# Kernel tuning notes

Measured on AMD Instinct MI355X. Metric: run time of the kernel, lower is better.

## Reference

```python
import jax, jax.numpy as jnp
import numpy as np

N = 100000   # number of nodes
H = 512      # n_hidden
K = 128      # number of clusters
BETA = 100.0 # cluster_temp
ALPHA = 0.5
NUM_ITER = 10
EPS = 1e-8


def _cluster(data, mu, cluster_temp, num_iter):
    """Differentiable soft k-means, faithful to cluster() in the torch source."""
    data = data / (jnp.linalg.norm(data, axis=1) + EPS)[:, None]
    dist = data @ mu.T  # placeholder; overwritten in loop (num_iter >= 1)
    for _ in range(num_iter):
        mu = mu / jnp.linalg.norm(mu, axis=1)[:, None]
        dist = data @ mu.T                      # [N, K]
        r = jax.nn.softmax(cluster_temp * dist, axis=1)
        cluster_r = r.sum(axis=0)               # [K]
        mu = (r.T @ data) / cluster_r[:, None]  # diag(1/cluster_r) @ (r.T @ data)
    r = jax.nn.softmax(cluster_temp * dist, axis=1)
    return mu, r


def setup_inputs() -> dict:
    key = jax.random.key(0)
    k1, k2, k3, k4 = jax.random.split(key, 4)
    positive = jax.random.normal(k1, (N, H), dtype=jnp.float32)
    negative = jax.random.normal(k2, (N, H), dtype=jnp.float32)
    init = jax.random.uniform(k3, (K, H), dtype=jnp.float32)  # torch.rand(K, nout)
    bound = 1.0 / np.sqrt(H)
    W = jax.random.uniform(k4, (H, H), dtype=jnp.float32, minval=-bound, maxval=bound)
    return {"positive": positive, "negative": negative, "init": init, "W": W}


def reference(positive, negative, init, W):
    # Clusterator.forward: 10-iter k-means, then 1 more iter from detached means
    mu_init, _ = _cluster(positive, init, BETA, NUM_ITER)
    mu, r = _cluster(positive, jax.lax.stop_gradient(mu_init), BETA, 1)

    graph_summary = jax.nn.sigmoid(positive.mean(axis=0))    # [H]
    cluster_summary = jax.nn.sigmoid(r @ mu)                 # [N, H]

    # Discriminator: features @ (W @ summary)
    Ws = W @ graph_summary                                    # [H]
    pos_graph = positive @ Ws                                 # [N]
    neg_graph = negative @ Ws                                 # [N]

    # BCEWithLogitsLoss with all-ones / all-zeros targets
    bce_ones = lambda x: jnp.mean(jax.nn.softplus(-x))
    bce_zeros = lambda x: jnp.mean(jax.nn.softplus(x))

    l = ALPHA * (bce_ones(pos_graph) + bce_zeros(neg_graph))

    # DiscriminatorK: rowwise dot of features with cluster summary
    pos_cluster = jnp.sum(positive * cluster_summary, axis=1)  # [N]
    neg_cluster = jnp.sum(negative * cluster_summary, axis=1)  # [N]

    l = l + (1.0 - ALPHA) * (bce_ones(pos_cluster) + bce_zeros(neg_cluster))
    return l
```

## Files before the change

### kernel.cpp

```cpp
#include <hip/hip_runtime.h>
#include <math.h>

#define NN 100000
#define PADN 100096
#define NBLK128 782
#define HH 512
#define KK 128
#define BETA 100.0f
#define EPSF 1e-8f
#define ITERS 11
#define NSPLIT 128
#define NCHUNK2 (PADN / 128)
#define PREPB 1024

typedef __attribute__((ext_vector_type(8))) short short8v;
typedef __attribute__((ext_vector_type(4))) float float4v;

typedef const __attribute__((address_space(1))) void* gas_t;
typedef __attribute__((address_space(3))) void* las_t;

__device__ __forceinline__ void gload16(const void* g, void* l) {
  __builtin_amdgcn_global_load_lds((gas_t)g, (las_t)l, 16, 0, 0);
}

__device__ __forceinline__ unsigned short f2bf(float x) {
  unsigned int u = __float_as_uint(x);
  unsigned int r = (u + 0x7fff + ((u >> 16) & 1)) >> 16;
  return (unsigned short)r;
}
__device__ __forceinline__ float bf2f(unsigned short b) {
  return __uint_as_float((unsigned int)b << 16);
}
__device__ __forceinline__ unsigned char f2fp8(float x) {
  return (unsigned char)(__builtin_amdgcn_cvt_pk_fp8_f32(x, x, 0, false) & 0xff);
}
__device__ __forceinline__ float fp82f(unsigned char b) {
  return __builtin_amdgcn_cvt_f32_fp8((unsigned int)b, 0);
}
#define CVT8_FP8(dst, pv)                                      \
  dst[0] = __builtin_amdgcn_cvt_f32_fp8((pv).x, 0);            \
  dst[1] = __builtin_amdgcn_cvt_f32_fp8((pv).x, 1);            \
  dst[2] = __builtin_amdgcn_cvt_f32_fp8((pv).x, 2);            \
  dst[3] = __builtin_amdgcn_cvt_f32_fp8((pv).x, 3);            \
  dst[4] = __builtin_amdgcn_cvt_f32_fp8((pv).y, 0);            \
  dst[5] = __builtin_amdgcn_cvt_f32_fp8((pv).y, 1);            \
  dst[6] = __builtin_amdgcn_cvt_f32_fp8((pv).y, 2);            \
  dst[7] = __builtin_amdgcn_cvt_f32_fp8((pv).y, 3);

__device__ __forceinline__ float wave_reduce_sum(float v) {
#pragma unroll
  for (int off = 32; off > 0; off >>= 1) v += __shfl_xor(v, off);
  return v;
}
__device__ __forceinline__ float softplusf(float x) {
  return fmaxf(x, 0.0f) + log1pf(expf(-fabsf(x)));
}

__global__ void prep_kernel(const float* __restrict__ pos,
                            float* __restrict__ inv_norm,
                            float* __restrict__ colpart,
                            unsigned short* __restrict__ posbb,
                            unsigned char* __restrict__ posb8) {
  int t = threadIdx.x;
  int w = t >> 6, lane = t & 63;
  int gw = blockIdx.x * 4 + w;
  float cpart[8] = {0, 0, 0, 0, 0, 0, 0, 0};
  for (int row = gw; row < NN; row += PREPB * 4) {
    const float* p = pos + (size_t)row * HH + lane * 8;
    float4 f0 = *(const float4*)p;
    float4 f1 = *(const float4*)(p + 4);
    float v[8] = {f0.x, f0.y, f0.z, f0.w, f1.x, f1.y, f1.z, f1.w};
    float ss = 0.f;
#pragma unroll
    for (int u = 0; u < 8; ++u) {
      ss += v[u] * v[u];
      cpart[u] += v[u];
    }
    ss = wave_reduce_sum(ss);
    float inv = 1.0f / (sqrtf(ss) + EPSF);
    if (lane == 0) inv_norm[row] = inv;
    short8v o;
#pragma unroll
    for (int u = 0; u < 8; ++u) o[u] = (short)f2bf(v[u] * inv);
    *(short8v*)&posbb[(size_t)row * HH + lane * 8] = o;
    int p0 = 0, p1 = 0;
    p0 = __builtin_amdgcn_cvt_pk_fp8_f32(v[0] * inv, v[1] * inv, p0, false);
    p0 = __builtin_amdgcn_cvt_pk_fp8_f32(v[2] * inv, v[3] * inv, p0, true);
    p1 = __builtin_amdgcn_cvt_pk_fp8_f32(v[4] * inv, v[5] * inv, p1, false);
    p1 = __builtin_amdgcn_cvt_pk_fp8_f32(v[6] * inv, v[7] * inv, p1, true);
    int2 pk = {p0, p1};
    *(int2*)&posb8[(size_t)row * HH + lane * 8] = pk;
  }
  {
    int idx = blockIdx.x * 256 + t;
    if (idx < (PADN - NN) * HH / 8) {
      short8v z = (short8v){0, 0, 0, 0, 0, 0, 0, 0};
      *(short8v*)&posbb[(size_t)NN * HH + idx * 8] = z;
    }
    if (idx < (PADN - NN) * HH / 16) {
      int4 z4 = {0, 0, 0, 0};
      *(int4*)&posb8[(size_t)NN * HH + idx * 16] = z4;
    }
  }
  __shared__ float cs[HH];
  cs[t] = 0.f;
  cs[t + 256] = 0.f;
  __syncthreads();
#pragma unroll
  for (int u = 0; u < 8; ++u) atomicAdd(&cs[lane * 8 + u], cpart[u]);
  __syncthreads();
  colpart[(size_t)blockIdx.x * HH + t] = cs[t];
  colpart[(size_t)blockIdx.x * HH + t + 256] = cs[t + 256];
}

__launch_bounds__(256)
__global__ void transpose_kernel(const unsigned short* __restrict__ posbb,
                                 unsigned char* __restrict__ posbT8) {
  __shared__ unsigned short tile[64][72];
  int t = threadIdx.x;
  int i0 = blockIdx.x * 64, h0 = blockIdx.y * 64;
  int r = t >> 2, cq = (t & 3) * 16;
#pragma unroll
  for (int q = 0; q < 2; ++q) {
    short8v v = *(const short8v*)&posbb[(size_t)(i0 + r) * HH + h0 + cq + q * 8];
#pragma unroll
    for (int e = 0; e < 8; ++e) tile[cq + q * 8 + e][r] = (unsigned short)v[e];
  }
  __syncthreads();
  int h = t >> 2, iq = (t & 3) * 16;
  const unsigned short* src = &tile[h][iq];
  int o[4];
#pragma unroll
  for (int q = 0; q < 4; ++q) {
    int pk = 0;
    pk = __builtin_amdgcn_cvt_pk_fp8_f32(bf2f(src[q * 4 + 0]), bf2f(src[q * 4 + 1]), pk, false);
    pk = __builtin_amdgcn_cvt_pk_fp8_f32(bf2f(src[q * 4 + 2]), bf2f(src[q * 4 + 3]), pk, true);
    o[q] = pk;
  }
  int4 ov = {o[0], o[1], o[2], o[3]};
  *(int4*)&posbT8[(size_t)(h0 + h) * PADN + i0 + iq] = ov;
}

__global__ void gs_kernel(const float* __restrict__ colpart, float* __restrict__ gs) {
  int t = threadIdx.x;
  float s = 0.f;
  for (int b = 0; b < PREPB; ++b) s += colpart[(size_t)b * HH + t];
  float m = s * (1.0f / NN);
  gs[t] = 1.0f / (1.0f + expf(-m));
}

__global__ void wsum_kernel(const float* __restrict__ W, const float* __restrict__ gs,
                            float* __restrict__ Ws) {
  int w = threadIdx.x >> 6, lane = threadIdx.x & 63;
  int row = blockIdx.x * 4 + w;
  const float* Wr = W + (size_t)row * HH;
  float s = 0.f;
#pragma unroll
  for (int j = 0; j < 8; ++j) s += Wr[lane + 64 * j] * gs[lane + 64 * j];
  s = wave_reduce_sum(s);
  if (lane == 0) Ws[row] = s;
}

__global__ void norm_mu_kernel(const float* __restrict__ src, unsigned char* __restrict__ mub8) {
  int k = blockIdx.x, t = threadIdx.x;
  float v0 = src[k * HH + t], v1 = src[k * HH + t + 256];
  float ss = v0 * v0 + v1 * v1;
  ss = wave_reduce_sum(ss);
  __shared__ float red[4];
  if ((t & 63) == 0) red[t >> 6] = ss;
  __syncthreads();
  float inv = 1.0f / sqrtf(red[0] + red[1] + red[2] + red[3]);
  mub8[k * HH + t] = f2fp8(v0 * inv);
  mub8[k * HH + t + 256] = f2fp8(v1 * inv);
}

__launch_bounds__(256, 4)
__global__ void dist_mfma(const unsigned char* __restrict__ posb8,
                          const unsigned char* __restrict__ mub8,
                          unsigned char* __restrict__ rbf8,
                          unsigned char* __restrict__ rbfT8,
                          float* __restrict__ crblk,
                          int write_rbf) {
  __shared__ __align__(16) unsigned char smem[32768];
  unsigned char* As0 = smem;
  unsigned char* Bs0 = smem + 16384;
  unsigned char* rT8 = smem;
  __shared__ float redM[2][128];
  __shared__ float redS[2][128];
  __shared__ float crS[2][128];

  int t = threadIdx.x;
  int w = t >> 6, l = t & 63;
  int wr = w >> 1, wc = w & 1;
  int i0 = blockIdx.x * 128;

  float4v acc[4][4];
#pragma unroll
  for (int mi = 0; mi < 4; ++mi)
#pragma unroll
    for (int ni = 0; ni < 4; ++ni) acc[mi][ni] = (float4v){0.f, 0.f, 0.f, 0.f};

  int rsub = l >> 2;
  int sslot = ((l & 3) ^ (rsub & 3)) << 4;

  auto stage = [&](int buf, int ch) {
    int h0 = ch * 64;
#pragma unroll
    for (int j = 0; j < 2; ++j) {
      int v = w * 2 + j;
      int row = v * 16 + rsub;
      gload16(posb8 + (size_t)(i0 + row) * HH + h0 + sslot, As0 + buf * 8192 + v * 1024);
      gload16(mub8 + (size_t)row * HH + h0 + sslot, Bs0 + buf * 8192 + v * 1024);
    }
  };

  stage(0, 0);
  int cur = 0;
  int g = l >> 4;
  int half8 = (g & 1) * 8;
  for (int ch = 0; ch < 8; ++ch) {
    if (ch < 7) {
      stage(cur ^ 1, ch + 1);
      asm volatile("s_waitcnt vmcnt(4)" ::: "memory");
    } else {
      asm volatile("s_waitcnt vmcnt(0)" ::: "memory");
    }
    __builtin_amdgcn_s_barrier();
    __builtin_amdgcn_sched_barrier(0);
    const char* ab = (const char*)(As0 + cur * 8192);
    const char* bb = (const char*)(Bs0 + cur * 8192);
#pragma unroll
    for (int ks = 0; ks < 2; ++ks) {
      long af[4], bfr[4];
      int slot16 = ks * 2 + (g >> 1);
      int soff = ((slot16 ^ (l & 3)) << 4) + half8;
#pragma unroll
      for (int mi = 0; mi < 4; ++mi) {
        int row = wr * 64 + mi * 16 + (l & 15);
        af[mi] = *(const long*)(ab + row * 64 + soff);
      }
#pragma unroll
      for (int ni = 0; ni < 4; ++ni) {
        int row = wc * 64 + ni * 16 + (l & 15);
        bfr[ni] = *(const long*)(bb + row * 64 + soff);
      }
#pragma unroll
      for (int mi = 0; mi < 4; ++mi)
#pragma unroll
        for (int ni = 0; ni < 4; ++ni)
          acc[mi][ni] = __builtin_amdgcn_mfma_f32_16x16x32_fp8_fp8(af[mi], bfr[ni], acc[mi][ni], 0, 0, 0);
    }
    __builtin_amdgcn_sched_barrier(0);
    __builtin_amdgcn_s_barrier();
    __builtin_amdgcn_sched_barrier(0);
    cur ^= 1;
  }

  float wmax[4][4];
#pragma unroll
  for (int mi = 0; mi < 4; ++mi)
#pragma unroll
    for (int j = 0; j < 4; ++j) {
      float m = fmaxf(fmaxf(acc[mi][0][j], acc[mi][1][j]), fmaxf(acc[mi][2][j], acc[mi][3][j])) * BETA;
      m = fmaxf(m, __shfl_xor(m, 1));
      m = fmaxf(m, __shfl_xor(m, 2));
      m = fmaxf(m, __shfl_xor(m, 4));
      m = fmaxf(m, __shfl_xor(m, 8));
      wmax[mi][j] = m;
    }
  if ((l & 15) == 0) {
#pragma unroll
    for (int mi = 0; mi < 4; ++mi)
#pragma unroll
      for (int j = 0; j < 4; ++j)
        redM[wc][wr * 64 + mi * 16 + (l >> 4) * 4 + j] = wmax[mi][j];
  }
  __syncthreads();
  float fm[4][4];
#pragma unroll
  for (int mi = 0; mi < 4; ++mi)
#pragma unroll
    for (int j = 0; j < 4; ++j) {
      int row = wr * 64 + mi * 16 + (l >> 4) * 4 + j;
      fm[mi][j] = fmaxf(redM[0][row], redM[1][row]);
    }
#pragma unroll
  for (int mi = 0; mi < 4; ++mi)
#pragma unroll
    for (int j = 0; j < 4; ++j) {
      float s = 0.f;
#pragma unroll
      for (int ni = 0; ni < 4; ++ni) {
        float e = __expf(acc[mi][ni][j] * BETA - fm[mi][j]);
        acc[mi][ni][j] = e;
        s += e;
      }
      s += __shfl_xor(s, 1);
      s += __shfl_xor(s, 2);
      s += __shfl_xor(s, 4);
      s += __shfl_xor(s, 8);
      wmax[mi][j] = s;
    }
  if ((l & 15) == 0) {
#pragma unroll
    for (int mi = 0; mi < 4; ++mi)
#pragma unroll
      for (int j = 0; j < 4; ++j)
        redS[wc][wr * 64 + mi * 16 + (l >> 4) * 4 + j] = wmax[mi][j];
  }
  __syncthreads();

  float cpart[4] = {0.f, 0.f, 0.f, 0.f};
#pragma unroll
  for (int mi = 0; mi < 4; ++mi)
#pragma unroll
    for (int j = 0; j < 4; ++j) {
      int row = wr * 64 + mi * 16 + (l >> 4) * 4 + j;
      float invs = 1.0f / (redS[0][row] + redS[1][row]);
      bool valid = (i0 + row) < NN;
#pragma unroll
      for (int ni = 0; ni < 4; ++ni) {
        unsigned char q8 = f2fp8(acc[mi][ni][j] * invs);
        if (valid) cpart[ni] += fp82f(q8);
        rT8[(wc * 64 + ni * 16 + (l & 15)) * 144 + row] = q8;
      }
    }
#pragma unroll
  for (int ni = 0; ni < 4; ++ni) {
    float c = cpart[ni];
    c += __shfl_xor(c, 16);
    c += __shfl_xor(c, 32);
    if (l < 16) crS[wr][wc * 64 + ni * 16 + l] = c;
  }
  __syncthreads();
  if (t < 128) crblk[(size_t)blockIdx.x * KK + t] = crS[0][t] + crS[1][t];

  {
    int c = t >> 1, half = t & 1;
    const unsigned char* src = &rT8[c * 144 + half * 64];
    unsigned char* dst = &rbfT8[(size_t)c * PADN + i0 + half * 64];
#pragma unroll
    for (int q = 0; q < 4; ++q)
      *(short8v*)(dst + q * 16) = *(const short8v*)(src + q * 16);
  }
  if (write_rbf) {
    int i = t >> 1, chalf = t & 1;
#pragma unroll
    for (int q = 0; q < 8; ++q) {
      unsigned int lo = 0, hi = 0;
#pragma unroll
      for (int e = 0; e < 4; ++e)
        lo |= ((unsigned int)rT8[(chalf * 64 + q * 8 + e) * 144 + i]) << (8 * e);
#pragma unroll
      for (int e = 0; e < 4; ++e)
        hi |= ((unsigned int)rT8[(chalf * 64 + q * 8 + 4 + e) * 144 + i]) << (8 * e);
      uint2 pk = {lo, hi};
      *(uint2*)&rbf8[(size_t)(i0 + i) * KK + chalf * 64 + q * 8] = pk;
    }
  }
}

__launch_bounds__(256, 2)
__global__ void muup_mfma(const unsigned char* __restrict__ rbfT8,
                          const unsigned char* __restrict__ posbT8,
                          unsigned short* __restrict__ part) {
  __shared__ __align__(16) unsigned char smem[65536];
  unsigned char* As0 = smem;
  unsigned char* Bs0 = smem + 32768;
  int t = threadIdx.x;
  int w = t >> 6, l = t & 63;
  int wr = w >> 1, wc = w & 1;
  int ht = blockIdx.x, s = blockIdx.y;

  float4v acc[4][4];
#pragma unroll
  for (int mi = 0; mi < 4; ++mi)
#pragma unroll
    for (int ni = 0; ni < 4; ++ni) acc[mi][ni] = (float4v){0.f, 0.f, 0.f, 0.f};

  int rsub = l >> 3;
  int sslot = ((l & 7) ^ rsub) << 4;

  auto stage = [&](int buf, int ch) {
    size_t ib = (size_t)ch * 128;
#pragma unroll
    for (int j = 0; j < 4; ++j) {
      int v = w * 4 + j;
      int row = v * 8 + rsub;
      gload16(rbfT8 + (size_t)row * PADN + ib + sslot, As0 + buf * 16384 + v * 1024);
      gload16(posbT8 + (size_t)(ht * 128 + row) * PADN + ib + sslot, Bs0 + buf * 16384 + v * 1024);
    }
  };

  int ch = s;
  stage(0, ch);
  int cur = 0;
  int g = l >> 4;
  int half8 = (g & 1) * 8;
  for (; ch < NCHUNK2; ch += NSPLIT) {
    int nxt = ch + NSPLIT;
    if (nxt < NCHUNK2) {
      stage(cur ^ 1, nxt);
      asm volatile("s_waitcnt vmcnt(8)" ::: "memory");
    } else {
      asm volatile("s_waitcnt vmcnt(0)" ::: "memory");
    }
    __builtin_amdgcn_s_barrier();
    __builtin_amdgcn_sched_barrier(0);
    const char* ab = (const char*)(As0 + cur * 16384);
    const char* bb = (const char*)(Bs0 + cur * 16384);
#pragma unroll
    for (int ks = 0; ks < 4; ++ks) {
      long af[4], bfr[4];
      int slot16 = ks * 2 + (g >> 1);
#pragma unroll
      for (int mi = 0; mi < 4; ++mi) {
        int row = wr * 64 + mi * 16 + (l & 15);
        af[mi] = *(const long*)(ab + row * 128 + ((slot16 ^ (l & 7)) << 4) + half8);
      }
#pragma unroll
      for (int ni = 0; ni < 4; ++ni) {
        int row = wc * 64 + ni * 16 + (l & 15);
        bfr[ni] = *(const long*)(bb + row * 128 + ((slot16 ^ (l & 7)) << 4) + half8);
      }
#pragma unroll
      for (int mi = 0; mi < 4; ++mi)
#pragma unroll
        for (int ni = 0; ni < 4; ++ni)
          acc[mi][ni] = __builtin_amdgcn_mfma_f32_16x16x32_fp8_fp8(af[mi], bfr[ni], acc[mi][ni], 0, 0, 0);
    }
    __builtin_amdgcn_sched_barrier(0);
    __builtin_amdgcn_s_barrier();
    __builtin_amdgcn_sched_barrier(0);
    cur ^= 1;
  }
#pragma unroll
  for (int mi = 0; mi < 4; ++mi)
#pragma unroll
    for (int ni = 0; ni < 4; ++ni)
#pragma unroll
      for (int j = 0; j < 4; ++j) {
        int c = wr * 64 + mi * 16 + (l >> 4) * 4 + j;
        int hh = wc * 64 + ni * 16 + (l & 15);
        part[((size_t)s * KK + c) * HH + ht * 128 + hh] = f2bf(acc[mi][ni][j]);
      }
}

__global__ void finorm_kernel(const unsigned short* __restrict__ part,
                              const float* __restrict__ crblk,
                              unsigned char* __restrict__ mub8,
                              unsigned char* __restrict__ mubT8, int write_mubT) {
  int c = blockIdx.x, t = threadIdx.x;
  __shared__ float credL[4];
  float crp = 0.f;
  for (int b = t; b < NBLK128; b += 256) crp += crblk[(size_t)b * KK + c];
  crp = wave_reduce_sum(crp);
  if ((t & 63) == 0) credL[t >> 6] = crp;
  __syncthreads();
  float cr = credL[0] + credL[1] + credL[2] + credL[3];
  float inv = 1.0f / cr;
  float s0 = 0.f, s1 = 0.f;
  const unsigned short* pb = part + (size_t)c * HH;
#pragma unroll 4
  for (int s2 = 0; s2 < NSPLIT; ++s2) {
    s0 += bf2f(pb[(size_t)s2 * KK * HH + t]);
    s1 += bf2f(pb[(size_t)s2 * KK * HH + t + 256]);
  }
  float v0 = s0 * inv, v1 = s1 * inv;
  if (write_mubT) {
    mubT8[(size_t)t * KK + c] = f2fp8(v0);
    mubT8[(size_t)(t + 256) * KK + c] = f2fp8(v1);
  }
  float ss = v0 * v0 + v1 * v1;
  ss = wave_reduce_sum(ss);
  __shared__ float red[4];
  if ((t & 63) == 0) red[t >> 6] = ss;
  __syncthreads();
  float rn = 1.0f / sqrtf(red[0] + red[1] + red[2] + red[3]);
  mub8[c * HH + t] = f2fp8(v0 * rn);
  mub8[c * HH + t + 256] = f2fp8(v1 * rn);
}

__launch_bounds__(512, 4)
__global__ void loss_mfma(const unsigned char* __restrict__ rbf8,
                          const unsigned char* __restrict__ mubT8,
                          const unsigned char* __restrict__ posb8,
                          const float* __restrict__ neg,
                          const float* __restrict__ inv_norm,
                          const float* __restrict__ Wsv, float* __restrict__ loss_accum) {
  __shared__ __align__(16) unsigned char rS8[128 * 128];
  __shared__ __align__(16) unsigned char BsU8[128 * 144];
  __shared__ float WsS[HH];
  __shared__ float pcS[128], ncS[128], pgS[128], ngS[128];
  int t = threadIdx.x;
  int w = t >> 6, l = t & 63;
  int wr = w >> 1, wc = w & 1;
  int i0 = blockIdx.x * 128;

  int rsub = l >> 3;
  int sslot = ((l & 7) ^ rsub) << 4;
  {
    const unsigned char* gb = rbf8 + (size_t)i0 * KK;
#pragma unroll
    for (int j = 0; j < 2; ++j) {
      int v = w * 2 + j;
      int row = v * 8 + rsub;
      gload16(gb + (size_t)row * KK + sslot, rS8 + v * 1024);
    }
  }
  WsS[t] = Wsv[t];
  if (t < 128) {
    pcS[t] = 0.f; ncS[t] = 0.f; pgS[t] = 0.f; ngS[t] = 0.f;
  }

  int g = l >> 4;
  int half8 = (g & 1) * 8;
  for (int p = 0; p < 4; ++p) {
    __syncthreads();
    {
      const unsigned char* gb = mubT8 + (size_t)p * 128 * KK;
#pragma unroll
      for (int j = 0; j < 2; ++j) {
        int v = w * 2 + j;
        int row = v * 8 + rsub;
        gload16(gb + (size_t)row * KK + sslot, BsU8 + v * 1024);
      }
    }
    __syncthreads();

    float4v acc[2][4];
#pragma unroll
    for (int mi = 0; mi < 2; ++mi)
#pragma unroll
      for (int ni = 0; ni < 4; ++ni) acc[mi][ni] = (float4v){0.f, 0.f, 0.f, 0.f};

#pragma unroll
    for (int ks = 0; ks < 4; ++ks) {
      long af[2], bfr[4];
      int slot16 = ks * 2 + (g >> 1);
      int soff = ((slot16 ^ (l & 7)) << 4) + half8;
#pragma unroll
      for (int mi = 0; mi < 2; ++mi) {
        int row = wr * 32 + mi * 16 + (l & 15);
        af[mi] = *(const long*)((const char*)rS8 + row * 128 + soff);
      }
#pragma unroll
      for (int ni = 0; ni < 4; ++ni) {
        int hrow = wc * 64 + ni * 16 + (l & 15);
        bfr[ni] = *(const long*)((const char*)BsU8 + hrow * 128 + soff);
      }
#pragma unroll
      for (int mi = 0; mi < 2; ++mi)
#pragma unroll
        for (int ni = 0; ni < 4; ++ni)
          acc[mi][ni] = __builtin_amdgcn_mfma_f32_16x16x32_fp8_fp8(af[mi], bfr[ni], acc[mi][ni], 0, 0, 0);
    }
    __syncthreads();

    unsigned char* csS = BsU8;
#pragma unroll
    for (int mi = 0; mi < 2; ++mi)
#pragma unroll
      for (int ni = 0; ni < 4; ++ni)
#pragma unroll
        for (int j = 0; j < 4; ++j) {
          int row = wr * 32 + mi * 16 + (l >> 4) * 4 + j;
          int col = wc * 64 + ni * 16 + (l & 15);
          csS[row * 144 + col] = f2fp8(1.0f / (1.0f + __expf(-acc[mi][ni][j])));
        }
    __syncthreads();

    {
      int rl = t >> 2;
      int q = t & 3;
      int gi = i0 + rl;
      bool valid = gi < NN;
      float pc = 0.f, nc = 0.f, pg = 0.f, ng = 0.f;
      const unsigned char* pr = posb8 + (size_t)gi * HH + p * 128;
      const float* nr = neg + (size_t)gi * HH + p * 128;
      const unsigned char* cr = csS + rl * 144;
#pragma unroll
      for (int e = 0; e < 4; ++e) {
        int cb = e * 32 + q * 8;
        uint2 cs8 = *(const uint2*)(cr + cb);
        if (valid) {
          uint2 pv8 = *(const uint2*)(pr + cb);
          float4 nv0 = *(const float4*)(nr + cb);
          float4 nv1 = *(const float4*)(nr + cb + 4);
          float sf[8], pf[8];
          CVT8_FP8(sf, cs8)
          CVT8_FP8(pf, pv8)
#pragma unroll
          for (int u = 0; u < 8; ++u) {
            float nv = (u < 4) ? (&nv0.x)[u] : (&nv1.x)[u - 4];
            float wv = WsS[p * 128 + cb + u];
            pc = fmaf(sf[u], pf[u], pc);
            nc = fmaf(sf[u], nv, nc);
            pg = fmaf(wv, pf[u], pg);
            ng = fmaf(wv, nv, ng);
          }
        }
      }
      pc += __shfl_xor(pc, 1); pc += __shfl_xor(pc, 2);
      nc += __shfl_xor(nc, 1); nc += __shfl_xor(nc, 2);
      pg += __shfl_xor(pg, 1); pg += __shfl_xor(pg, 2);
      ng += __shfl_xor(ng, 1); ng += __shfl_xor(ng, 2);
      if (q == 0) {
        pcS[rl] += pc;
        ncS[rl] += nc;
        pgS[rl] += pg;
        ngS[rl] += ng;
      }
    }
  }
  __syncthreads();
  if (t < 128) {
    int gi = i0 + t;
    float contrib = 0.f;
    if (gi < NN) {
      float nrm = 1.0f / inv_norm[gi];
      float pg = pgS[t] * nrm;
      float pc = pcS[t] * nrm;
      float ng = ngS[t];
      float nc = ncS[t];
      contrib = 0.5f * (softplusf(-pg) + softplusf(ng)) +
                0.5f * (softplusf(-pc) + softplusf(nc));
    }
    contrib = wave_reduce_sum(contrib);
    if (l == 0) atomicAdd(loss_accum, contrib);
  }
}

__global__ void out_kernel(const float* __restrict__ loss_accum, float* __restrict__ out) {
  out[0] = loss_accum[0] * (1.0f / NN);
}

extern "C" void kernel_launch(void* const* d_in, const int* in_sizes, int n_in,
                              void* d_out, int out_size, void* d_ws, size_t ws_size,
                              hipStream_t stream) {
  const float* pos = (const float*)d_in[0];
  const float* neg = (const float*)d_in[1];
  const float* init = (const float*)d_in[2];
  const float* W = (const float*)d_in[3];
  float* out = (float*)d_out;

  char* ws = (char*)d_ws;
  size_t off = 0;
  auto alloc = [&](size_t bytes) {
    void* p = ws + off;
    off = (off + bytes + 255) & ~(size_t)255;
    return p;
  };
  unsigned char* posb8 = (unsigned char*)alloc((size_t)PADN * HH);
  unsigned short* posbb = (unsigned short*)alloc((size_t)PADN * HH * 2);
  unsigned char* posbT8 = (unsigned char*)alloc((size_t)HH * PADN);
  unsigned char* rbf8 = (unsigned char*)alloc((size_t)PADN * KK);
  unsigned char* rbfT8 = (unsigned char*)alloc((size_t)KK * PADN);
  unsigned short* part = (unsigned short*)alloc((size_t)NSPLIT * KK * HH * 2);
  float* colpart = (float*)alloc((size_t)PREPB * HH * 4);
  float* crblk = (float*)alloc((size_t)NBLK128 * KK * 4);
  float* inv_norm = (float*)alloc((size_t)NN * 4);
  unsigned char* mub8 = (unsigned char*)alloc((size_t)KK * HH);
  unsigned char* mubT8 = (unsigned char*)alloc((size_t)KK * HH);
  float* gs = (float*)alloc(HH * 4);
  float* Ws = (float*)alloc(HH * 4);
  float* loss_accum = (float*)alloc(16);

  hipMemsetAsync(loss_accum, 0, sizeof(float), stream);

  prep_kernel<<<PREPB, 256, 0, stream>>>(pos, inv_norm, colpart, posbb, posb8);
  transpose_kernel<<<dim3(PADN / 64, HH / 64), 256, 0, stream>>>(posbb, posbT8);
  gs_kernel<<<1, 512, 0, stream>>>(colpart, gs);
  wsum_kernel<<<128, 256, 0, stream>>>(W, gs, Ws);

  norm_mu_kernel<<<KK, 256, 0, stream>>>(init, mub8);
  for (int it = 0; it < ITERS; ++it) {
    dist_mfma<<<NBLK128, 256, 0, stream>>>(posb8, mub8, rbf8, rbfT8, crblk, it == ITERS - 1 ? 1 : 0);
    muup_mfma<<<dim3(4, NSPLIT), 256, 0, stream>>>(rbfT8, posbT8, part);
    finorm_kernel<<<KK, 256, 0, stream>>>(part, crblk, mub8, mubT8, it == ITERS - 1 ? 1 : 0);
  }

  loss_mfma<<<NBLK128, 512, 0, stream>>>(rbf8, mubT8, posb8, neg, inv_norm, Ws, loss_accum);
  out_kernel<<<1, 1, 0, stream>>>(loss_accum, out);
}
```

Measured before the change: 964.7 us.

## Store mu partials in fp8 and split loss into cs GEMM plus streaming pass

Per-split mu-update partial sums are now stored as fp8 instead of bf16, halving the partial-buffer traffic between muup and finorm each iteration. The fused loss kernel is split into a cs_mfma kernel, which computes sigmoid(r@mu) tiles into an fp8 N×H buffer, and a separate loss_stream kernel that reads that buffer along with pos and neg rows and reduces the loss. The split aims for better GEMM tiling and occupancy, at the cost of an extra ~50MB write and read. fp8 partials summed over 128 splits risk noticeable accuracy loss in the cluster means.

```diff
diff --git a/kernel.cpp b/kernel.cpp
--- a/kernel.cpp
+++ b/kernel.cpp
@@ -363,7 +363,7 @@
 __launch_bounds__(256, 2)
 __global__ void muup_mfma(const unsigned char* __restrict__ rbfT8,
                           const unsigned char* __restrict__ posbT8,
-                          unsigned short* __restrict__ part) {
+                          unsigned char* __restrict__ part8) {
   __shared__ __align__(16) unsigned char smem[65536];
   unsigned char* As0 = smem;
   unsigned char* Bs0 = smem + 32768;
@@ -442,11 +442,11 @@
       for (int j = 0; j < 4; ++j) {
         int c = wr * 64 + mi * 16 + (l >> 4) * 4 + j;
         int hh = wc * 64 + ni * 16 + (l & 15);
-        part[((size_t)s * KK + c) * HH + ht * 128 + hh] = f2bf(acc[mi][ni][j]);
-      }
-}
-
-__global__ void finorm_kernel(const unsigned short* __restrict__ part,
+        part8[((size_t)s * KK + c) * HH + ht * 128 + hh] = f2fp8(acc[mi][ni][j]);
+      }
+}
+
+__global__ void finorm_kernel(const unsigned char* __restrict__ part8,
                               const float* __restrict__ crblk,
                               unsigned char* __restrict__ mub8,
                               unsigned char* __restrict__ mubT8, int write_mubT) {
@@ -460,11 +460,11 @@
   float cr = credL[0] + credL[1] + credL[2] + credL[3];
   float inv = 1.0f / cr;
   float s0 = 0.f, s1 = 0.f;
-  const unsigned short* pb = part + (size_t)c * HH;
+  const unsigned char* pb = part8 + (size_t)c * HH;
 #pragma unroll 4
   for (int s2 = 0; s2 < NSPLIT; ++s2) {
-    s0 += bf2f(pb[(size_t)s2 * KK * HH + t]);
-    s1 += bf2f(pb[(size_t)s2 * KK * HH + t + 256]);
+    s0 += fp82f(pb[(size_t)s2 * KK * HH + t]);
+    s1 += fp82f(pb[(size_t)s2 * KK * HH + t + 256]);
   }
   float v0 = s0 * inv, v1 = s1 * inv;
   if (write_mubT) {
@@ -481,154 +481,137 @@
   mub8[c * HH + t + 256] = f2fp8(v1 * rn);
 }
 
-__launch_bounds__(512, 4)
-__global__ void loss_mfma(const unsigned char* __restrict__ rbf8,
-                          const unsigned char* __restrict__ mubT8,
-                          const unsigned char* __restrict__ posb8,
-                          const float* __restrict__ neg,
-                          const float* __restrict__ inv_norm,
-                          const float* __restrict__ Wsv, float* __restrict__ loss_accum) {
-  __shared__ __align__(16) unsigned char rS8[128 * 128];
-  __shared__ __align__(16) unsigned char BsU8[128 * 144];
-  __shared__ float WsS[HH];
-  __shared__ float pcS[128], ncS[128], pgS[128], ngS[128];
+__launch_bounds__(256, 4)
+__global__ void cs_mfma(const unsigned char* __restrict__ rbf8,
+                        const unsigned char* __restrict__ mubT8,
+                        unsigned char* __restrict__ cs8) {
+  __shared__ __align__(16) unsigned char smem[32768];
+  unsigned char* As = smem;
+  unsigned char* Bs = smem + 16384;
+  unsigned char* ct = smem;
   int t = threadIdx.x;
   int w = t >> 6, l = t & 63;
   int wr = w >> 1, wc = w & 1;
   int i0 = blockIdx.x * 128;
+  int h0 = blockIdx.y * 128;
 
   int rsub = l >> 3;
   int sslot = ((l & 7) ^ rsub) << 4;
   {
-    const unsigned char* gb = rbf8 + (size_t)i0 * KK;
-#pragma unroll
-    for (int j = 0; j < 2; ++j) {
-      int v = w * 2 + j;
+    const unsigned char* ga = rbf8 + (size_t)i0 * KK;
+    const unsigned char* gb = mubT8 + (size_t)h0 * KK;
+#pragma unroll
+    for (int j = 0; j < 4; ++j) {
+      int v = w * 4 + j;
       int row = v * 8 + rsub;
-      gload16(gb + (size_t)row * KK + sslot, rS8 + v * 1024);
-    }
-  }
-  WsS[t] = Wsv[t];
-  if (t < 128) {
-    pcS[t] = 0.f; ncS[t] = 0.f; pgS[t] = 0.f; ngS[t] = 0.f;
-  }
+      gload16(ga + (size_t)row * KK + sslot, As + v * 1024);
+      gload16(gb + (size_t)row * KK + sslot, Bs + v * 1024);
+    }
+  }
+  __syncthreads();
+
+  float4v acc[4][4];
+#pragma unroll
+  for (int mi = 0; mi < 4; ++mi)
+#pragma unroll
+    for (int ni = 0; ni < 4; ++ni) acc[mi][ni] = (float4v){0.f, 0.f, 0.f, 0.f};
 
   int g = l >> 4;
   int half8 = (g & 1) * 8;
-  for (int p = 0; p < 4; ++p) {
-    __syncthreads();
-    {
-      const unsigned char* gb = mubT8 + (size_t)p * 128 * KK;
-#pragma unroll
-      for (int j = 0; j < 2; ++j) {
-        int v = w * 2 + j;
-        int row = v * 8 + rsub;
-        gload16(gb + (size_t)row * KK + sslot, BsU8 + v * 1024);
-      }
-    }
-    __syncthreads();
-
-    float4v acc[2][4];
-#pragma unroll
-    for (int mi = 0; mi < 2; ++mi)
-#pragma unroll
-      for (int ni = 0; ni < 4; ++ni) acc[mi][ni] = (float4v){0.f, 0.f, 0.f, 0.f};
-
-#pragma unroll
-    for (int ks = 0; ks < 4; ++ks) {
-      long af[2], bfr[4];
-      int slot16 = ks * 2 + (g >> 1);
-      int soff = ((slot16 ^ (l & 7)) << 4) + half8;
-#pragma unroll
-      for (int mi = 0; mi < 2; ++mi) {
-        int row = wr * 32 + mi * 16 + (l & 15);
-        af[mi] = *(const long*)((const char*)rS8 + row * 128 + soff);
-      }
-#pragma unroll
-      for (int ni = 0; ni < 4; ++ni) {
-        int hrow = wc * 64 + ni * 16 + (l & 15);
-        bfr[ni] = *(const long*)((const char*)BsU8 + hrow * 128 + soff);
-      }
-#pragma unroll
-      for (int mi = 0; mi < 2; ++mi)
-#pragma unroll
-        for (int ni = 0; ni < 4; ++ni)
-          acc[mi][ni] = __builtin_amdgcn_mfma_f32_16x16x32_fp8_fp8(af[mi], bfr[ni], acc[mi][ni], 0, 0, 0);
-    }
-    __syncthreads();
-
-    unsigned char* csS = BsU8;
-#pragma unroll
-    for (int mi = 0; mi < 2; ++mi)
+#pragma unroll
+  for (int ks = 0; ks < 4; ++ks) {
+    long af[4], bfr[4];
+    int slot16 = ks * 2 + (g >> 1);
+    int soff = ((slot16 ^ (l & 7)) << 4) + half8;
+#pragma unroll
+    for (int mi = 0; mi < 4; ++mi) {
+      int row = wr * 64 + mi * 16 + (l & 15);
+      af[mi] = *(const long*)((const char*)As + row * 128 + soff);
+    }
+#pragma unroll
+    for (int ni = 0; ni < 4; ++ni) {
+      int row = wc * 64 + ni * 16 + (l & 15);
+      bfr[ni] = *(const long*)((const char*)Bs + row * 128 + soff);
+    }
+#pragma unroll
+    for (int mi = 0; mi < 4; ++mi)
 #pragma unroll
       for (int ni = 0; ni < 4; ++ni)
-#pragma unroll
-        for (int j = 0; j < 4; ++j) {
-          int row = wr * 32 + mi * 16 + (l >> 4) * 4 + j;
-          int col = wc * 64 + ni * 16 + (l & 15);
-          csS[row * 144 + col] = f2fp8(1.0f / (1.0f + __expf(-acc[mi][ni][j])));
-        }
-    __syncthreads();
-
-    {
-      int rl = t >> 2;
-      int q = t & 3;
-      int gi = i0 + rl;
-      bool valid = gi < NN;
-      float pc = 0.f, nc = 0.f, pg = 0.f, ng = 0.f;
-      const unsigned char* pr = posb8 + (size_t)gi * HH + p * 128;
-      const float* nr = neg + (size_t)gi * HH + p * 128;
-      const unsigned char* cr = csS + rl * 144;
-#pragma unroll
-      for (int e = 0; e < 4; ++e) {
-        int cb = e * 32 + q * 8;
-        uint2 cs8 = *(const uint2*)(cr + cb);
-        if (valid) {
-          uint2 pv8 = *(const uint2*)(pr + cb);
-          float4 nv0 = *(const float4*)(nr + cb);
-          float4 nv1 = *(const float4*)(nr + cb + 4);
-          float sf[8], pf[8];
-          CVT8_FP8(sf, cs8)
-          CVT8_FP8(pf, pv8)
-#pragma unroll
-          for (int u = 0; u < 8; ++u) {
-            float nv = (u < 4) ? (&nv0.x)[u] : (&nv1.x)[u - 4];
-            float wv = WsS[p * 128 + cb + u];
-            pc = fmaf(sf[u], pf[u], pc);
-            nc = fmaf(sf[u], nv, nc);
-            pg = fmaf(wv, pf[u], pg);
-            ng = fmaf(wv, nv, ng);
-          }
-        }
-      }
-      pc += __shfl_xor(pc, 1); pc += __shfl_xor(pc, 2);
-      nc += __shfl_xor(nc, 1); nc += __shfl_xor(nc, 2);
-      pg += __shfl_xor(pg, 1); pg += __shfl_xor(pg, 2);
-      ng += __shfl_xor(ng, 1); ng += __shfl_xor(ng, 2);
-      if (q == 0) {
-        pcS[rl] += pc;
-        ncS[rl] += nc;
-        pgS[rl] += pg;
-        ngS[rl] += ng;
-      }
-    }
-  }
-  __syncthreads();
-  if (t < 128) {
-    int gi = i0 + t;
-    float contrib = 0.f;
-    if (gi < NN) {
-      float nrm = 1.0f / inv_norm[gi];
-      float pg = pgS[t] * nrm;
-      float pc = pcS[t] * nrm;
-      float ng = ngS[t];
-      float nc = ncS[t];
-      contrib = 0.5f * (softplusf(-pg) + softplusf(ng)) +
-                0.5f * (softplusf(-pc) + softplusf(nc));
-    }
-    contrib = wave_reduce_sum(contrib);
-    if (l == 0) atomicAdd(loss_accum, contrib);
-  }
+        acc[mi][ni] = __builtin_amdgcn_mfma_f32_16x16x32_fp8_fp8(af[mi], bfr[ni], acc[mi][ni], 0, 0, 0);
+  }
+  __syncthreads();
+
+#pragma unroll
+  for (int mi = 0; mi < 4; ++mi)
+#pragma unroll
+    for (int ni = 0; ni < 4; ++ni)
+#pragma unroll
+      for (int j = 0; j < 4; ++j) {
+        int row = wr * 64 + mi * 16 + (l >> 4) * 4 + j;
+        int col = wc * 64 + ni * 16 + (l & 15);
+        ct[row * 144 + col] = f2fp8(1.0f / (1.0f + __expf(-acc[mi][ni][j])));
+      }
+  __syncthreads();
+
+  {
+    int r2 = t >> 1, half = t & 1;
+    const unsigned char* src = ct + r2 * 144 + half * 64;
+    unsigned char* dst = cs8 + (size_t)(i0 + r2) * HH + h0 + half * 64;
+#pragma unroll
+    for (int q = 0; q < 4; ++q)
+      *(short8v*)(dst + q * 16) = *(const short8v*)(src + q * 16);
+  }
+}
+
+__launch_bounds__(256)
+__global__ void loss_stream(const unsigned char* __restrict__ cs8,
+                            const unsigned char* __restrict__ posb8,
+                            const float* __restrict__ neg,
+                            const float* __restrict__ inv_norm,
+                            const float* __restrict__ Wsv,
+                            float* __restrict__ loss_accum) {
+  __shared__ float WsS[HH];
+  __shared__ float bred[4];
+  int t = threadIdx.x;
+  WsS[t] = Wsv[t];
+  WsS[t + 256] = Wsv[t + 256];
+  __syncthreads();
+  int w = t >> 6, l = t & 63;
+  float total = 0.f;
+  for (int row = blockIdx.x * 4 + w; row < NN; row += 2048 * 4) {
+    const unsigned char* cr = cs8 + (size_t)row * HH + l * 8;
+    const unsigned char* pr = posb8 + (size_t)row * HH + l * 8;
+    const float* nr = neg + (size_t)row * HH + l * 8;
+    uint2 c8 = *(const uint2*)cr;
+    uint2 p8 = *(const uint2*)pr;
+    float4 n0 = *(const float4*)nr;
+    float4 n1 = *(const float4*)(nr + 4);
+    float sf[8], pf[8];
+    CVT8_FP8(sf, c8)
+    CVT8_FP8(pf, p8)
+    float pc = 0.f, nc = 0.f, pg = 0.f, ng = 0.f;
+#pragma unroll
+    for (int u = 0; u < 8; ++u) {
+      float nv = (u < 4) ? (&n0.x)[u] : (&n1.x)[u - 4];
+      float wv = WsS[l * 8 + u];
+      pc = fmaf(sf[u], pf[u], pc);
+      nc = fmaf(sf[u], nv, nc);
+      pg = fmaf(wv, pf[u], pg);
+      ng = fmaf(wv, nv, ng);
+    }
+    pc = wave_reduce_sum(pc);
+    nc = wave_reduce_sum(nc);
+    pg = wave_reduce_sum(pg);
+    ng = wave_reduce_sum(ng);
+    if (l == 0) {
+      float nrm = 1.0f / inv_norm[row];
+      total += 0.5f * (softplusf(-pg * nrm) + softplusf(ng)) +
+               0.5f * (softplusf(-pc * nrm) + softplusf(nc));
+    }
+  }
+  if (l == 0) bred[w] = total;
+  __syncthreads();
+  if (t == 0) atomicAdd(loss_accum, bred[0] + bred[1] + bred[2] + bred[3]);
 }
 
 __global__ void out_kernel(const float* __restrict__ loss_accum, float* __restrict__ out) {
@@ -656,7 +639,8 @@
   unsigned char* posbT8 = (unsigned char*)alloc((size_t)HH * PADN);
   unsigned char* rbf8 = (unsigned char*)alloc((size_t)PADN * KK);
   unsigned char* rbfT8 = (unsigned char*)alloc((size_t)KK * PADN);
-  unsigned short* part = (unsigned short*)alloc((size_t)NSPLIT * KK * HH * 2);
+  unsigned char* cs8 = (unsigned char*)alloc((size_t)PADN * HH);
+  unsigned char* part8 = (unsigned char*)alloc((size_t)NSPLIT * KK * HH);
   float* colpart = (float*)alloc((size_t)PREPB * HH * 4);
   float* crblk = (float*)alloc((size_t)NBLK128 * KK * 4);
   float* inv_norm = (float*)alloc((size_t)NN * 4);
@@ -676,10 +660,11 @@
   norm_mu_kernel<<<KK, 256, 0, stream>>>(init, mub8);
   for (int it = 0; it < ITERS; ++it) {
     dist_mfma<<<NBLK128, 256, 0, stream>>>(posb8, mub8, rbf8, rbfT8, crblk, it == ITERS - 1 ? 1 : 0);
-    muup_mfma<<<dim3(4, NSPLIT), 256, 0, stream>>>(rbfT8, posbT8, part);
-    finorm_kernel<<<KK, 256, 0, stream>>>(part, crblk, mub8, mubT8, it == ITERS - 1 ? 1 : 0);
-  }
-
-  loss_mfma<<<NBLK128, 512, 0, stream>>>(rbf8, mubT8, posb8, neg, inv_norm, Ws, loss_accum);
+    muup_mfma<<<dim3(4, NSPLIT), 256, 0, stream>>>(rbfT8, posbT8, part8);
+    finorm_kernel<<<KK, 256, 0, stream>>>(part8, crblk, mub8, mubT8, it == ITERS - 1 ? 1 : 0);
+  }
+
+  cs_mfma<<<dim3(NBLK128, 4), 256, 0, stream>>>(rbf8, mubT8, cs8);
+  loss_stream<<<2048, 256, 0, stream>>>(cs8, posb8, neg, inv_norm, Ws, loss_accum);
   out_kernel<<<1, 1, 0, stream>>>(loss_accum, out);
 }
```

New measurement: 990.4 us. 2.7% more time.
